# Kernel optimization log

Hardware: AMD Instinct MI355X
Metric: run time of the kernel (lower is better)

The kernel has to match this reference:

```python
import jax, jax.numpy as jnp
import numpy as np

N, E, D, H = 100000, 200000, 384, 768
BN_EPS = 1e-5


def setup_inputs() -> dict:
    key = jax.random.key(0)
    ks = jax.random.split(key, 8)
    w = lambda k, sh: jax.random.normal(k, sh, jnp.float32) * 0.02
    return {
        "x": jax.random.normal(ks[0], (N, D), jnp.float32),
        "edge_attr": jax.random.normal(ks[1], (E, D), jnp.float32),
        "gamma": jnp.ones((D,), jnp.float32),
        "beta": jnp.zeros((D,), jnp.float32),
        "eps": jnp.zeros((), jnp.float32),          # GINE train_eps, init 0
        "W_edge": w(ks[2], (D, D)),
        "b_edge": jnp.zeros((D,), jnp.float32),
        "W1": w(ks[3], (D, H)),
        "b1": jnp.zeros((H,), jnp.float32),
        "W2": w(ks[4], (H, D)),
        "b2": jnp.zeros((D,), jnp.float32),
        "edge_index": jax.random.randint(ks[5], (2, E), 0, N, jnp.int32),
    }


def reference(x, edge_attr, gamma, beta, eps, W_edge, b_edge, W1, b1, W2, b2, edge_index):
    # BatchNorm1d over the node (batch) dimension, training statistics
    mu = jnp.mean(x, axis=0)
    var = jnp.var(x, axis=0)
    h = (x - mu) * jax.lax.rsqrt(var + BN_EPS) * gamma + beta  # [N, D]

    src, dst = edge_index[0], edge_index[1]  # j -> i (PyG source_to_target)
    # GINEConv message: relu(x_j + lin(edge_attr))
    msg = jax.nn.relu(h[src] + edge_attr @ W_edge + b_edge)     # [E, D]
    agg = jax.ops.segment_sum(msg, dst, num_segments=N)         # sum aggregation

    # nn((1+eps)*x_i + agg) where nn = Linear->GELU->Linear
    z = (1.0 + eps) * h + agg
    z = jax.nn.gelu(z @ W1 + b1, approximate=False) @ W2 + b2

    # residual + outer GELU activation (drop_path/dropout = identity at eval)
    return x + jax.nn.gelu(z, approximate=False)
```

## Files before the change

### kernel.cpp

```cpp
#include <hip/hip_runtime.h>
#include <hip/hip_bf16.h>

#define Df 384
#define Hf 768
#define SCAN_CH 4096

typedef __bf16 bf16x8 __attribute__((ext_vector_type(8)));
typedef float f32x4 __attribute__((ext_vector_type(4)));

struct __attribute__((aligned(4))) U12 { unsigned int x, y, z; };

__device__ inline unsigned short f2bf(float f) {
    __hip_bfloat16 h = __float2bfloat16(f);
    return __builtin_bit_cast(unsigned short, h);
}
__device__ inline float bf2f(unsigned short u) {
    unsigned int v = ((unsigned int)u) << 16;
    return __builtin_bit_cast(float, v);
}
__device__ inline float lobf(unsigned int v) { return bf2f((unsigned short)(v & 0xffff)); }
__device__ inline float hibf(unsigned int v) { return bf2f((unsigned short)(v >> 16)); }
__device__ inline unsigned int pk2(float a, float b) {
    return (unsigned int)f2bf(a) | ((unsigned int)f2bf(b) << 16);
}
__device__ inline float gelu_(float v) {
    return 0.5f * v * (1.0f + erff(v * 0.70710678118654752f));
}
__device__ inline void gload16(const void* g, void* l) {
    __builtin_amdgcn_global_load_lds(
        (const __attribute__((address_space(1))) unsigned int*)g,
        (__attribute__((address_space(3))) unsigned int*)l, 16, 0, 0);
}

__global__ void bn_stats(const float* __restrict__ x, float* __restrict__ stats, int N) {
    int t = threadIdx.x;
    int c4 = (t % 96) * 4;
    int rs = t / 96;
    float s0 = 0, s1 = 0, s2 = 0, s3 = 0, q0 = 0, q1 = 0, q2 = 0, q3 = 0;
    for (int r = blockIdx.x * 2 + rs; r < N; r += gridDim.x * 2) {
        float4 v = *(const float4*)(x + (size_t)r * Df + c4);
        s0 += v.x; s1 += v.y; s2 += v.z; s3 += v.w;
        q0 += v.x * v.x; q1 += v.y * v.y; q2 += v.z * v.z; q3 += v.w * v.w;
    }
    unsafeAtomicAdd(&stats[c4 + 0], s0);
    unsafeAtomicAdd(&stats[c4 + 1], s1);
    unsafeAtomicAdd(&stats[c4 + 2], s2);
    unsafeAtomicAdd(&stats[c4 + 3], s3);
    unsafeAtomicAdd(&stats[Df + c4 + 0], q0);
    unsafeAtomicAdd(&stats[Df + c4 + 1], q1);
    unsafeAtomicAdd(&stats[Df + c4 + 2], q2);
    unsafeAtomicAdd(&stats[Df + c4 + 3], q3);
}

__global__ void bn_finalize(const float* __restrict__ stats,
                            const float* __restrict__ gamma,
                            const float* __restrict__ beta,
                            float* __restrict__ coef, int N) {
    int c = threadIdx.x;
    float invN = 1.0f / (float)N;
    float mu = stats[c] * invN;
    float var = stats[Df + c] * invN - mu * mu;
    float rs = rsqrtf(var + 1e-5f);
    float a = gamma[c] * rs;
    coef[c] = a;
    coef[Df + c] = beta[c] - mu * a;
}

__global__ void h_kernel(const float* __restrict__ x, const float* __restrict__ coef,
                         unsigned short* __restrict__ hb, int tot8) {
    int i = blockIdx.x * 256 + threadIdx.x;
    if (i >= tot8) return;
    size_t base = (size_t)i * 8;
    int c = (int)(base % Df);
    float4 x0 = *(const float4*)(x + base);
    float4 x1 = *(const float4*)(x + base + 4);
    const float* a = coef + c;
    const float* b = coef + Df + c;
    uint4 o;
    o.x = pk2(x0.x * a[0] + b[0], x0.y * a[1] + b[1]);
    o.y = pk2(x0.z * a[2] + b[2], x0.w * a[3] + b[3]);
    o.z = pk2(x1.x * a[4] + b[4], x1.y * a[5] + b[5]);
    o.w = pk2(x1.z * a[6] + b[6], x1.w * a[7] + b[7]);
    *(uint4*)(hb + base) = o;
}

__global__ void cast_bf16(const float* __restrict__ src, unsigned short* __restrict__ dst, int tot8) {
    int i = blockIdx.x * 256 + threadIdx.x;
    if (i >= tot8) return;
    size_t base = (size_t)i * 8;
    float4 x0 = *(const float4*)(src + base);
    float4 x1 = *(const float4*)(src + base + 4);
    uint4 o;
    o.x = pk2(x0.x, x0.y); o.y = pk2(x0.z, x0.w);
    o.z = pk2(x1.x, x1.y); o.w = pk2(x1.z, x1.w);
    *(uint4*)(dst + base) = o;
}

__global__ void wtrans(const float* __restrict__ Wsrc, unsigned short* __restrict__ Wdst,
                       int K, int Nc) {
    int idx = blockIdx.x * 256 + threadIdx.x;
    if (idx >= K * Nc) return;
    int k = idx / Nc, n = idx % Nc;
    Wdst[(size_t)n * K + k] = f2bf(Wsrc[idx]);
}

__global__ void degree_k(const int* __restrict__ dst, int* __restrict__ deg, int E) {
    int e = blockIdx.x * 256 + threadIdx.x;
    if (e < E) atomicAdd(&deg[dst[e]], 1);
}

__global__ void scan1(const int* __restrict__ deg, int* __restrict__ off,
                      int* __restrict__ sums, int N) {
    __shared__ int ts[256];
    int t = threadIdx.x;
    int base = blockIdx.x * SCAN_CH + t * 16;
    int v[16];
    int s = 0;
    for (int j = 0; j < 16; j++) {
        int idx = base + j;
        int d = (idx < N) ? deg[idx] : 0;
        v[j] = s;
        s += d;
    }
    ts[t] = s;
    __syncthreads();
    for (int o = 1; o < 256; o <<= 1) {
        int add = (t >= o) ? ts[t - o] : 0;
        __syncthreads();
        ts[t] += add;
        __syncthreads();
    }
    int pre = t ? ts[t - 1] : 0;
    for (int j = 0; j < 16; j++) {
        int idx = base + j;
        if (idx < N) off[idx] = pre + v[j];
    }
    if (t == 255) sums[blockIdx.x] = ts[255];
}

__global__ void scan2(int* __restrict__ sums, int nb) {
    int acc = 0;
    for (int b = 0; b < nb; b++) { int v = sums[b]; sums[b] = acc; acc += v; }
    sums[nb] = acc;
}

__global__ void scan3(int* __restrict__ off, const int* __restrict__ sums, int N, int nb) {
    int idx = blockIdx.x * 256 + threadIdx.x;
    if (idx < N) off[idx] += sums[idx / SCAN_CH];
    else if (idx == N) off[N] = sums[nb];
}

__global__ void fill_k(const int* __restrict__ dst, const int* __restrict__ src,
                       int* __restrict__ cursor, int* __restrict__ srcp,
                       int* __restrict__ pose, int E) {
    int e = blockIdx.x * 256 + threadIdx.x;
    if (e >= E) return;
    int pos = atomicAdd(&cursor[dst[e]], 1);
    srcp[pos] = src[e];
    pose[e] = pos;
}

__global__ __launch_bounds__(256) void aggregate(
    const unsigned short* __restrict__ msgl, const unsigned short* __restrict__ hb,
    const int* __restrict__ off, const int* __restrict__ srcp,
    const float* __restrict__ epsp,
    unsigned short* __restrict__ zb, int N) {
    int lane = threadIdx.x & 63;
    int wid = threadIdx.x >> 6;
    int nwaves = gridDim.x * 4;
    float s1p = 1.0f + epsp[0];
    int loff = lane * 6;
    for (int i = blockIdx.x * 4 + wid; i < N; i += nwaves) {
        int o0 = off[i], o1 = off[i + 1];
        float a0 = 0, a1 = 0, a2 = 0, a3 = 0, a4 = 0, a5 = 0;
        for (int p = o0; p < o1; ++p) {
            int s = srcp[p];
            U12 mv = *(const U12*)(msgl + (size_t)p * Df + loff);
            U12 hv = *(const U12*)(hb + (size_t)s * Df + loff);
            a0 += fmaxf(lobf(mv.x) + lobf(hv.x), 0.f);
            a1 += fmaxf(hibf(mv.x) + hibf(hv.x), 0.f);
            a2 += fmaxf(lobf(mv.y) + lobf(hv.y), 0.f);
            a3 += fmaxf(hibf(mv.y) + hibf(hv.y), 0.f);
            a4 += fmaxf(lobf(mv.z) + lobf(hv.z), 0.f);
            a5 += fmaxf(hibf(mv.z) + hibf(hv.z), 0.f);
        }
        U12 hv = *(const U12*)(hb + (size_t)i * Df + loff);
        U12 o;
        o.x = pk2(s1p * lobf(hv.x) + a0, s1p * hibf(hv.x) + a1);
        o.y = pk2(s1p * lobf(hv.y) + a2, s1p * hibf(hv.y) + a3);
        o.z = pk2(s1p * lobf(hv.z) + a4, s1p * hibf(hv.z) + a5);
        *(U12*)(zb + (size_t)i * Df + loff) = o;
    }
}

template <int NT, int EPI>
__global__ __launch_bounds__(512, 1) void gemm8(
    const unsigned short* __restrict__ Ab, const unsigned short* __restrict__ Bt,
    const float* __restrict__ bias, int M, int ncols,
    const int* __restrict__ pose,
    unsigned short* __restrict__ outb,
    const float* __restrict__ xres, float* __restrict__ outf, int ldo) {
    constexpr int K = NT * 64;
    __shared__ __align__(16) unsigned short As[3 * 256 * 64];
    __shared__ __align__(16) unsigned short Bs[3 * 128 * 64];

    const int t = threadIdx.x;
    const int nwg = gridDim.x;
    const int orig = blockIdx.x;
    const int xcd = orig & 7;
    const int q = nwg >> 3, r = nwg & 7;
    const int wgid = (xcd < r ? xcd * (q + 1) : r * (q + 1) + (xcd - r) * q) + (orig >> 3);
    const int pp = wgid / ncols;
    const int m0 = pp * 256;
    const int n0 = (wgid - pp * ncols) * 128;

    const int lane = t & 63;
    const int wid = t >> 6;
    const int fr = lane & 15;
    const int kg = lane >> 4;
    const int wm = wid >> 1;
    const int wn = wid & 1;
    const int srow = lane >> 3;
    const int scol = (lane & 7) ^ srow;

    f32x4 acc[4][4];
#pragma unroll
    for (int i = 0; i < 4; i++)
#pragma unroll
        for (int j = 0; j < 4; j++) acc[i][j] = (f32x4){0.f, 0.f, 0.f, 0.f};

#define STG_A(u, kt_, bufi) do {                                                \
        int rr_ = m0 + (u) * 64 + wid * 8 + srow;                               \
        if (rr_ >= M) rr_ = M - 1;                                              \
        gload16(Ab + (size_t)rr_ * K + (kt_) * 64 + (scol << 3),                \
                &As[(bufi) * 16384 + (u) * 4096 + wid * 512]);                  \
    } while (0)
#define STG_B(u, kt_, bufi) do {                                                \
        int rr_ = n0 + (u) * 64 + wid * 8 + srow;                               \
        gload16(Bt + (size_t)rr_ * K + (kt_) * 64 + (scol << 3),                \
                &Bs[(bufi) * 8192 + (u) * 4096 + wid * 512]);                   \
    } while (0)

#pragma unroll
    for (int u = 0; u < 4; u++) STG_A(u, 0, 0);
    STG_B(0, 0, 0); STG_B(1, 0, 0);
#pragma unroll
    for (int u = 0; u < 4; u++) STG_A(u, 1, 1);
    STG_B(0, 1, 1); STG_B(1, 1, 1);
    asm volatile("s_waitcnt vmcnt(6)" ::: "memory");
    __builtin_amdgcn_s_barrier();
    asm volatile("" ::: "memory");

    for (int kt = 0; kt < NT; ++kt) {
        const unsigned short* Ac = As + (kt % 3) * 16384;
        const unsigned short* Bc = Bs + (kt % 3) * 8192;
        const int nb = (kt + 2) % 3;
        const bool st = (kt + 2) < NT;

        if (st) { STG_A(0, kt + 2, nb); STG_A(1, kt + 2, nb); }

        bf16x8 a[4], b[4];
#pragma unroll
        for (int i = 0; i < 4; i++) {
            const int row = wm * 64 + i * 16 + fr;
            a[i] = *(const bf16x8*)&Ac[row * 64 + ((kg ^ (row & 7)) << 3)];
        }
#pragma unroll
        for (int j = 0; j < 4; j++) {
            const int row = wn * 64 + j * 16 + fr;
            b[j] = *(const bf16x8*)&Bc[row * 64 + ((kg ^ (row & 7)) << 3)];
        }
        if (st) { STG_A(2, kt + 2, nb); STG_A(3, kt + 2, nb); }
        __builtin_amdgcn_s_setprio(1);
#pragma unroll
        for (int i = 0; i < 4; i++)
#pragma unroll
            for (int j = 0; j < 4; j++)
                acc[i][j] = __builtin_amdgcn_mfma_f32_16x16x32_bf16(a[i], b[j], acc[i][j], 0, 0, 0);
        __builtin_amdgcn_s_setprio(0);

        if (st) { STG_B(0, kt + 2, nb); STG_B(1, kt + 2, nb); }
#pragma unroll
        for (int i = 0; i < 4; i++) {
            const int row = wm * 64 + i * 16 + fr;
            a[i] = *(const bf16x8*)&Ac[row * 64 + (((4 + kg) ^ (row & 7)) << 3)];
        }
#pragma unroll
        for (int j = 0; j < 4; j++) {
            const int row = wn * 64 + j * 16 + fr;
            b[j] = *(const bf16x8*)&Bc[row * 64 + (((4 + kg) ^ (row & 7)) << 3)];
        }
        __builtin_amdgcn_s_setprio(1);
#pragma unroll
        for (int i = 0; i < 4; i++)
#pragma unroll
            for (int j = 0; j < 4; j++)
                acc[i][j] = __builtin_amdgcn_mfma_f32_16x16x32_bf16(a[i], b[j], acc[i][j], 0, 0, 0);
        __builtin_amdgcn_s_setprio(0);

        if (kt < NT - 1) {
            if (st) asm volatile("s_waitcnt vmcnt(6)" ::: "memory");
            else    asm volatile("s_waitcnt vmcnt(0)" ::: "memory");
            __builtin_amdgcn_s_barrier();
            asm volatile("" ::: "memory");
        }
    }
#undef STG_A
#undef STG_B

    float bi[4];
#pragma unroll
    for (int j = 0; j < 4; j++) bi[j] = bias[n0 + wn * 64 + j * 16 + fr];

    const int kg4 = kg * 4;
#pragma unroll
    for (int i = 0; i < 4; i++) {
        const int rb = m0 + wm * 64 + i * 16 + kg4;
#pragma unroll
        for (int j = 0; j < 4; j++) {
            const int c = n0 + wn * 64 + j * 16 + fr;
#pragma unroll
            for (int r = 0; r < 4; r++) {
                const int row = rb + r;
                if (row < M) {
                    float v = acc[i][j][r] + bi[j];
                    if (EPI == 1) {
                        outb[(size_t)row * ldo + c] = f2bf(gelu_(v));
                    } else if (EPI == 2) {
                        size_t o = (size_t)row * ldo + c;
                        outf[o] = xres[o] + gelu_(v);
                    } else {
                        outb[(size_t)pose[row] * ldo + c] = f2bf(v);
                    }
                }
            }
        }
    }
}

extern "C" void kernel_launch(void* const* d_in, const int* in_sizes, int n_in,
                              void* d_out, int out_size, void* d_ws, size_t ws_size,
                              hipStream_t stream) {
    const float* x = (const float*)d_in[0];
    const float* ea = (const float*)d_in[1];
    const float* gamma = (const float*)d_in[2];
    const float* beta = (const float*)d_in[3];
    const float* epsp = (const float*)d_in[4];
    const float* W_edge = (const float*)d_in[5];
    const float* b_edge = (const float*)d_in[6];
    const float* W1 = (const float*)d_in[7];
    const float* b1 = (const float*)d_in[8];
    const float* W2 = (const float*)d_in[9];
    const float* b2 = (const float*)d_in[10];
    const int* eidx = (const int*)d_in[11];
    float* out = (float*)d_out;
    const int N = in_sizes[0] / Df;
    const int E = in_sizes[1] / Df;
    const int* esrc = eidx;
    const int* edst = eidx + E;

    char* w = (char*)d_ws;
    size_t off_ = 0;
    auto alloc = [&](size_t bytes) { char* p = w + off_; off_ += (bytes + 255) & ~(size_t)255; return p; };
    float* stats = (float*)alloc(2 * Df * sizeof(float));
    float* coef = (float*)alloc(2 * Df * sizeof(float));
    unsigned short* hb = (unsigned short*)alloc((size_t)N * Df * 2);
    unsigned short* zb = (unsigned short*)alloc((size_t)N * Df * 2);
    unsigned short* tb = (unsigned short*)alloc((size_t)N * Hf * 2);
    unsigned short* WeT = (unsigned short*)alloc((size_t)Df * Df * 2);
    unsigned short* W1T = (unsigned short*)alloc((size_t)Df * Hf * 2);
    unsigned short* W2T = (unsigned short*)alloc((size_t)Hf * Df * 2);
    int* deg = (int*)alloc((size_t)(N + 1) * 4);
    int* offs = (int*)alloc((size_t)(N + 1) * 4);
    int* srcp = (int*)alloc((size_t)E * 4);
    int* pose = (int*)alloc((size_t)E * 4);
    int* sums = (int*)alloc(64 * 4);
    size_t msgl_bytes = (size_t)E * Df * 2;
    unsigned short* msgl;
    if (off_ + msgl_bytes <= ws_size) msgl = (unsigned short*)alloc(msgl_bytes);
    else msgl = (unsigned short*)d_out;
    unsigned short* eab = tb;
    (void)n_in; (void)out_size;

    hipMemsetAsync(stats, 0, 2 * Df * sizeof(float), stream);
    hipMemsetAsync(deg, 0, (size_t)N * 4, stream);

    bn_stats<<<1024, 192, 0, stream>>>(x, stats, N);
    bn_finalize<<<1, Df, 0, stream>>>(stats, gamma, beta, coef, N);
    int tot8 = N * Df / 8;
    h_kernel<<<(tot8 + 255) / 256, 256, 0, stream>>>(x, coef, hb, tot8);

    int etot8 = E * Df / 8;
    cast_bf16<<<(etot8 + 255) / 256, 256, 0, stream>>>(ea, eab, etot8);

    wtrans<<<(Df * Df + 255) / 256, 256, 0, stream>>>(W_edge, WeT, Df, Df);
    wtrans<<<(Df * Hf + 255) / 256, 256, 0, stream>>>(W1, W1T, Df, Hf);
    wtrans<<<(Hf * Df + 255) / 256, 256, 0, stream>>>(W2, W2T, Hf, Df);

    int nb = (N + SCAN_CH - 1) / SCAN_CH;
    degree_k<<<(E + 255) / 256, 256, 0, stream>>>(edst, deg, E);
    scan1<<<nb, 256, 0, stream>>>(deg, offs, sums, N);
    scan2<<<1, 1, 0, stream>>>(sums, nb);
    scan3<<<(N + 256) / 256, 256, 0, stream>>>(offs, sums, N, nb);
    hipMemcpyAsync(deg, offs, (size_t)N * 4, hipMemcpyDeviceToDevice, stream);
    fill_k<<<(E + 255) / 256, 256, 0, stream>>>(edst, esrc, deg, srcp, pose, E);

    int ep = (E + 255) / 256;
    gemm8<6, 3><<<dim3(ep * (Df / 128)), 512, 0, stream>>>(
        eab, WeT, b_edge, E, Df / 128, pose, msgl, nullptr, nullptr, Df);

    aggregate<<<2048, 256, 0, stream>>>(msgl, hb, offs, srcp, epsp, zb, N);

    int np = (N + 255) / 256;
    gemm8<6, 1><<<dim3(np * (Hf / 128)), 512, 0, stream>>>(
        zb, W1T, b1, N, Hf / 128, nullptr, tb, nullptr, nullptr, Hf);
    gemm8<12, 2><<<dim3(np * (Df / 128)), 512, 0, stream>>>(
        tb, W2T, b2, N, Df / 128, nullptr, nullptr, x, out, Df);
}
```

Measured before the change: 1.121 ms.

## Widen GEMM tiles to 256x192 with half-K double-buffered ping-pong pipeline

Replaces the 256x128 triple-buffered GEMM with a 256x192 tile: each wave owns a 128x48 sub-tile and the K tile is split into two 32-wide halves in a double buffer. Loads for later stages are interleaved between MFMA phases, with barriers around each phase. The wider N tile is meant to cut how often A is re-fetched and to raise MFMA work per shared-memory read. In exchange it uses more registers for accumulators, adds many more barriers per K step, and launches fewer workgroups.

```diff
diff --git a/kernel.cpp b/kernel.cpp
--- a/kernel.cpp
+++ b/kernel.cpp
@@ -194,15 +194,15 @@
 }
 
 template <int NT, int EPI>
-__global__ __launch_bounds__(512, 1) void gemm8(
+__global__ __launch_bounds__(512, 1) void gemm8p(
     const unsigned short* __restrict__ Ab, const unsigned short* __restrict__ Bt,
     const float* __restrict__ bias, int M, int ncols,
     const int* __restrict__ pose,
     unsigned short* __restrict__ outb,
     const float* __restrict__ xres, float* __restrict__ outf, int ldo) {
     constexpr int K = NT * 64;
-    __shared__ __align__(16) unsigned short As[3 * 256 * 64];
-    __shared__ __align__(16) unsigned short Bs[3 * 128 * 64];
+    __shared__ __align__(16) unsigned short AS[2 * 2 * 256 * 32];
+    __shared__ __align__(16) unsigned short BS[2 * 2 * 192 * 32];
 
     const int t = threadIdx.x;
     const int nwg = gridDim.x;
@@ -212,118 +212,137 @@
     const int wgid = (xcd < r ? xcd * (q + 1) : r * (q + 1) + (xcd - r) * q) + (orig >> 3);
     const int pp = wgid / ncols;
     const int m0 = pp * 256;
-    const int n0 = (wgid - pp * ncols) * 128;
+    const int n0 = (wgid - pp * ncols) * 192;
 
     const int lane = t & 63;
     const int wid = t >> 6;
     const int fr = lane & 15;
     const int kg = lane >> 4;
-    const int wm = wid >> 1;
-    const int wn = wid & 1;
-    const int srow = lane >> 3;
-    const int scol = (lane & 7) ^ srow;
-
-    f32x4 acc[4][4];
-#pragma unroll
-    for (int i = 0; i < 4; i++)
-#pragma unroll
-        for (int j = 0; j < 4; j++) acc[i][j] = (f32x4){0.f, 0.f, 0.f, 0.f};
-
-#define STG_A(u, kt_, bufi) do {                                                \
-        int rr_ = m0 + (u) * 64 + wid * 8 + srow;                               \
-        if (rr_ >= M) rr_ = M - 1;                                              \
-        gload16(Ab + (size_t)rr_ * K + (kt_) * 64 + (scol << 3),                \
-                &As[(bufi) * 16384 + (u) * 4096 + wid * 512]);                  \
-    } while (0)
-#define STG_B(u, kt_, bufi) do {                                                \
-        int rr_ = n0 + (u) * 64 + wid * 8 + srow;                               \
-        gload16(Bt + (size_t)rr_ * K + (kt_) * 64 + (scol << 3),                \
-                &Bs[(bufi) * 8192 + (u) * 4096 + wid * 512]);                   \
-    } while (0)
-
-#pragma unroll
-    for (int u = 0; u < 4; u++) STG_A(u, 0, 0);
-    STG_B(0, 0, 0); STG_B(1, 0, 0);
-#pragma unroll
-    for (int u = 0; u < 4; u++) STG_A(u, 1, 1);
-    STG_B(0, 1, 1); STG_B(1, 1, 1);
+    const int wm = wid >> 2;
+    const int wn = wid & 3;
+    const int segw = ((lane & 3) ^ ((lane >> 3) & 3)) << 3;
+    const int rsw = (kg ^ ((fr >> 1) & 3)) << 3;
+
+    f32x4 acc[8][3];
+#pragma unroll
+    for (int i = 0; i < 8; i++)
+#pragma unroll
+        for (int j = 0; j < 3; j++) acc[i][j] = (f32x4){0.f, 0.f, 0.f, 0.f};
+
+#define STG_AH(tt, kh) do {                                                     \
+        const int bb_ = ((tt) & 1) * 2 + (kh);                                  \
+        _Pragma("unroll")                                                       \
+        for (int c_ = 0; c_ < 2; c_++) {                                        \
+            int row_ = c_ * 128 + wid * 16 + (lane >> 2);                       \
+            int gr_ = m0 + row_; if (gr_ >= M) gr_ = M - 1;                     \
+            gload16(Ab + (size_t)gr_ * K + (tt) * 64 + (kh) * 32 + segw,        \
+                    &AS[(bb_ * 256 + c_ * 128 + wid * 16) * 32]);               \
+        } } while (0)
+#define STG_BH(tt, kh) do {                                                     \
+        const int bb_ = ((tt) & 1) * 2 + (kh);                                  \
+        _Pragma("unroll")                                                       \
+        for (int c_ = 0; c_ < 2; c_++) {                                        \
+            int row_ = c_ * 64 + wid * 16 + (lane >> 2);                        \
+            gload16(Bt + (size_t)(n0 + row_) * K + (tt) * 64 + (kh) * 32 + segw,\
+                    &BS[(bb_ * 192 + c_ * 64 + wid * 16) * 32]);                \
+        } } while (0)
+
+    STG_AH(0, 0); STG_BH(0, 0); STG_AH(0, 1); STG_BH(0, 1);
+    STG_AH(1, 0); STG_BH(1, 0); STG_AH(1, 1);
     asm volatile("s_waitcnt vmcnt(6)" ::: "memory");
     __builtin_amdgcn_s_barrier();
-    asm volatile("" ::: "memory");
 
     for (int kt = 0; kt < NT; ++kt) {
-        const unsigned short* Ac = As + (kt % 3) * 16384;
-        const unsigned short* Bc = Bs + (kt % 3) * 8192;
-        const int nb = (kt + 2) % 3;
-        const bool st = (kt + 2) < NT;
-
-        if (st) { STG_A(0, kt + 2, nb); STG_A(1, kt + 2, nb); }
-
-        bf16x8 a[4], b[4];
-#pragma unroll
-        for (int i = 0; i < 4; i++) {
-            const int row = wm * 64 + i * 16 + fr;
-            a[i] = *(const bf16x8*)&Ac[row * 64 + ((kg ^ (row & 7)) << 3)];
+        const int b = kt & 1;
+        const unsigned short* Ah0 = &AS[(b * 2 + 0) * 256 * 32];
+        const unsigned short* Ah1 = &AS[(b * 2 + 1) * 256 * 32];
+        const unsigned short* Bh0 = &BS[(b * 2 + 0) * 192 * 32];
+        const unsigned short* Bh1 = &BS[(b * 2 + 1) * 192 * 32];
+        bf16x8 a[8], bf0, bf1, bf2;
+
+#pragma unroll
+        for (int i = 0; i < 8; i++)
+            a[i] = *(const bf16x8*)&Ah0[(wm * 128 + i * 16 + fr) * 32 + rsw];
+        bf0 = *(const bf16x8*)&Bh0[(wn * 48 + 0 + fr) * 32 + rsw];
+        bf1 = *(const bf16x8*)&Bh0[(wn * 48 + 16 + fr) * 32 + rsw];
+        if (kt + 1 < NT) STG_BH(kt + 1, 1);
+        __builtin_amdgcn_s_barrier();
+        asm volatile("s_waitcnt lgkmcnt(0)" ::: "memory");
+        __builtin_amdgcn_sched_barrier(0);
+        __builtin_amdgcn_s_setprio(1);
+#pragma unroll
+        for (int i = 0; i < 8; i++) {
+            acc[i][0] = __builtin_amdgcn_mfma_f32_16x16x32_bf16(a[i], bf0, acc[i][0], 0, 0, 0);
+            acc[i][1] = __builtin_amdgcn_mfma_f32_16x16x32_bf16(a[i], bf1, acc[i][1], 0, 0, 0);
         }
-#pragma unroll
-        for (int j = 0; j < 4; j++) {
-            const int row = wn * 64 + j * 16 + fr;
-            b[j] = *(const bf16x8*)&Bc[row * 64 + ((kg ^ (row & 7)) << 3)];
+        __builtin_amdgcn_s_setprio(0);
+        __builtin_amdgcn_s_barrier();
+
+        bf2 = *(const bf16x8*)&Bh0[(wn * 48 + 32 + fr) * 32 + rsw];
+        if (kt + 2 < NT) STG_AH(kt + 2, 0);
+        __builtin_amdgcn_s_barrier();
+        asm volatile("s_waitcnt lgkmcnt(0)" ::: "memory");
+        __builtin_amdgcn_sched_barrier(0);
+        __builtin_amdgcn_s_setprio(1);
+#pragma unroll
+        for (int i = 0; i < 8; i++)
+            acc[i][2] = __builtin_amdgcn_mfma_f32_16x16x32_bf16(a[i], bf2, acc[i][2], 0, 0, 0);
+        __builtin_amdgcn_s_setprio(0);
+        __builtin_amdgcn_s_barrier();
+
+#pragma unroll
+        for (int i = 0; i < 8; i++)
+            a[i] = *(const bf16x8*)&Ah1[(wm * 128 + i * 16 + fr) * 32 + rsw];
+        bf0 = *(const bf16x8*)&Bh1[(wn * 48 + 0 + fr) * 32 + rsw];
+        bf1 = *(const bf16x8*)&Bh1[(wn * 48 + 16 + fr) * 32 + rsw];
+        if (kt + 2 < NT) STG_BH(kt + 2, 0);
+        __builtin_amdgcn_s_barrier();
+        asm volatile("s_waitcnt lgkmcnt(0)" ::: "memory");
+        __builtin_amdgcn_sched_barrier(0);
+        __builtin_amdgcn_s_setprio(1);
+#pragma unroll
+        for (int i = 0; i < 8; i++) {
+            acc[i][0] = __builtin_amdgcn_mfma_f32_16x16x32_bf16(a[i], bf0, acc[i][0], 0, 0, 0);
+            acc[i][1] = __builtin_amdgcn_mfma_f32_16x16x32_bf16(a[i], bf1, acc[i][1], 0, 0, 0);
         }
-        if (st) { STG_A(2, kt + 2, nb); STG_A(3, kt + 2, nb); }
+        __builtin_amdgcn_s_setprio(0);
+        __builtin_amdgcn_s_barrier();
+
+        bf2 = *(const bf16x8*)&Bh1[(wn * 48 + 32 + fr) * 32 + rsw];
+        if (kt + 2 < NT) STG_AH(kt + 2, 1);
+        __builtin_amdgcn_s_barrier();
+        asm volatile("s_waitcnt lgkmcnt(0)" ::: "memory");
+        __builtin_amdgcn_sched_barrier(0);
         __builtin_amdgcn_s_setprio(1);
 #pragma unroll
-        for (int i = 0; i < 4; i++)
-#pragma unroll
-            for (int j = 0; j < 4; j++)
-                acc[i][j] = __builtin_amdgcn_mfma_f32_16x16x32_bf16(a[i], b[j], acc[i][j], 0, 0, 0);
+        for (int i = 0; i < 8; i++)
+            acc[i][2] = __builtin_amdgcn_mfma_f32_16x16x32_bf16(a[i], bf2, acc[i][2], 0, 0, 0);
         __builtin_amdgcn_s_setprio(0);
-
-        if (st) { STG_B(0, kt + 2, nb); STG_B(1, kt + 2, nb); }
-#pragma unroll
-        for (int i = 0; i < 4; i++) {
-            const int row = wm * 64 + i * 16 + fr;
-            a[i] = *(const bf16x8*)&Ac[row * 64 + (((4 + kg) ^ (row & 7)) << 3)];
+        if (kt + 1 < NT) {
+            if (kt + 2 < NT) asm volatile("s_waitcnt vmcnt(6)" ::: "memory");
+            else             asm volatile("s_waitcnt vmcnt(0)" ::: "memory");
         }
-#pragma unroll
-        for (int j = 0; j < 4; j++) {
-            const int row = wn * 64 + j * 16 + fr;
-            b[j] = *(const bf16x8*)&Bc[row * 64 + (((4 + kg) ^ (row & 7)) << 3)];
-        }
-        __builtin_amdgcn_s_setprio(1);
-#pragma unroll
-        for (int i = 0; i < 4; i++)
-#pragma unroll
-            for (int j = 0; j < 4; j++)
-                acc[i][j] = __builtin_amdgcn_mfma_f32_16x16x32_bf16(a[i], b[j], acc[i][j], 0, 0, 0);
-        __builtin_amdgcn_s_setprio(0);
-
-        if (kt < NT - 1) {
-            if (st) asm volatile("s_waitcnt vmcnt(6)" ::: "memory");
-            else    asm volatile("s_waitcnt vmcnt(0)" ::: "memory");
-            __builtin_amdgcn_s_barrier();
-            asm volatile("" ::: "memory");
-        }
-    }
-#undef STG_A
-#undef STG_B
-
-    float bi[4];
-#pragma unroll
-    for (int j = 0; j < 4; j++) bi[j] = bias[n0 + wn * 64 + j * 16 + fr];
+        __builtin_amdgcn_s_barrier();
+    }
+#undef STG_AH
+#undef STG_BH
+
+    float bi[3];
+#pragma unroll
+    for (int j = 0; j < 3; j++) bi[j] = bias[n0 + wn * 48 + j * 16 + fr];
 
     const int kg4 = kg * 4;
 #pragma unroll
-    for (int i = 0; i < 4; i++) {
-        const int rb = m0 + wm * 64 + i * 16 + kg4;
-#pragma unroll
-        for (int j = 0; j < 4; j++) {
-            const int c = n0 + wn * 64 + j * 16 + fr;
-#pragma unroll
-            for (int r = 0; r < 4; r++) {
-                const int row = rb + r;
+    for (int i = 0; i < 8; i++) {
+        const int rb = m0 + wm * 128 + i * 16 + kg4;
+#pragma unroll
+        for (int j = 0; j < 3; j++) {
+            const int c = n0 + wn * 48 + j * 16 + fr;
+#pragma unroll
+            for (int rr = 0; rr < 4; rr++) {
+                const int row = rb + rr;
                 if (row < M) {
-                    float v = acc[i][j][r] + bi[j];
+                    float v = acc[i][j][rr] + bi[j];
                     if (EPI == 1) {
                         outb[(size_t)row * ldo + c] = f2bf(gelu_(v));
                     } else if (EPI == 2) {
@@ -406,14 +425,14 @@
     fill_k<<<(E + 255) / 256, 256, 0, stream>>>(edst, esrc, deg, srcp, pose, E);
 
     int ep = (E + 255) / 256;
-    gemm8<6, 3><<<dim3(ep * (Df / 128)), 512, 0, stream>>>(
-        eab, WeT, b_edge, E, Df / 128, pose, msgl, nullptr, nullptr, Df);
+    gemm8p<6, 3><<<dim3(ep * (Df / 192)), 512, 0, stream>>>(
+        eab, WeT, b_edge, E, Df / 192, pose, msgl, nullptr, nullptr, Df);
 
     aggregate<<<2048, 256, 0, stream>>>(msgl, hb, offs, srcp, epsp, zb, N);
 
     int np = (N + 255) / 256;
-    gemm8<6, 1><<<dim3(np * (Hf / 128)), 512, 0, stream>>>(
-        zb, W1T, b1, N, Hf / 128, nullptr, tb, nullptr, nullptr, Hf);
-    gemm8<12, 2><<<dim3(np * (Df / 128)), 512, 0, stream>>>(
-        tb, W2T, b2, N, Df / 128, nullptr, nullptr, x, out, Df);
-}
+    gemm8p<6, 1><<<dim3(np * (Hf / 192)), 512, 0, stream>>>(
+        zb, W1T, b1, N, Hf / 192, nullptr, tb, nullptr, nullptr, Hf);
+    gemm8p<12, 2><<<dim3(np * (Df / 192)), 512, 0, stream>>>(
+        tb, W2T, b2, N, Df / 192, nullptr, nullptr, x, out, Df);
+}
```

New measurement: 1.277 ms. +13.8%, slower.

## Fuse MLP's two GEMMs into one kernel keeping hidden activations in LDS

Applied to the files above, without the earlier changes.

Replaces the two tiled GEMM launches for the node MLP with a single fused kernel. Each 64-row block stages its z tile in shared memory, computes the 768-wide GELU hidden layer into shared memory, then runs the second GEMM with the residual GELU epilogue. This avoids writing and rereading the N×768 bf16 hidden tensor in global memory. In exchange, weights are read straight from global or L2 on every k-step with no LDS staging or pipelining. The 144 KB of LDS also limits each CU to one block, which may cut MFMA efficiency compared with the tuned gemm8.

```diff
diff --git a/kernel.cpp b/kernel.cpp
--- a/kernel.cpp
+++ b/kernel.cpp
@@ -193,6 +193,124 @@
     }
 }
 
+__global__ __launch_bounds__(512, 1) void mlp_fused(
+    const unsigned short* __restrict__ zb, const unsigned short* __restrict__ W1T,
+    const float* __restrict__ b1, const unsigned short* __restrict__ W2T,
+    const float* __restrict__ b2, const float* __restrict__ x,
+    float* __restrict__ out, int M) {
+    __shared__ __align__(16) unsigned short zS[64 * 384];
+    __shared__ __align__(16) unsigned short tS[64 * 768];
+
+    const int t = threadIdx.x;
+    const int lane = t & 63;
+    const int wid = t >> 6;
+    const int fr = lane & 15;
+    const int kg = lane >> 4;
+    const int kg4 = kg * 4;
+    const int m0 = blockIdx.x * 64;
+
+#pragma unroll
+    for (int si = 0; si < 6; si++) {
+        int c = (wid * 6 + si) * 64 + lane;
+        int row = c / 48;
+        int pos = c - row * 48;
+        int gr = m0 + row; if (gr >= M) gr = M - 1;
+        gload16(zb + (size_t)gr * Df + ((pos ^ (row & 7)) << 3),
+                &zS[(wid * 6 + si) * 512]);
+    }
+    asm volatile("s_waitcnt vmcnt(0)" ::: "memory");
+    __builtin_amdgcn_s_barrier();
+
+    const int cb1 = wid * 96;
+    f32x4 acc1[4][6];
+#pragma unroll
+    for (int i = 0; i < 4; i++)
+#pragma unroll
+        for (int j = 0; j < 6; j++) acc1[i][j] = (f32x4){0.f, 0.f, 0.f, 0.f};
+
+#pragma unroll
+    for (int kt = 0; kt < 12; kt++) {
+        bf16x8 a[4], b[6];
+#pragma unroll
+        for (int i = 0; i < 4; i++) {
+            const int rr = i * 16 + fr;
+            const int pos = (kt * 4 + kg) ^ (rr & 7);
+            a[i] = *(const bf16x8*)&zS[rr * Df + pos * 8];
+        }
+#pragma unroll
+        for (int j = 0; j < 6; j++)
+            b[j] = *(const bf16x8*)(W1T + (size_t)(cb1 + j * 16 + fr) * Df + kt * 32 + kg * 8);
+#pragma unroll
+        for (int i = 0; i < 4; i++)
+#pragma unroll
+            for (int j = 0; j < 6; j++)
+                acc1[i][j] = __builtin_amdgcn_mfma_f32_16x16x32_bf16(a[i], b[j], acc1[i][j], 0, 0, 0);
+    }
+
+    float bv1[6];
+#pragma unroll
+    for (int j = 0; j < 6; j++) bv1[j] = b1[cb1 + j * 16 + fr];
+#pragma unroll
+    for (int i = 0; i < 4; i++) {
+#pragma unroll
+        for (int j = 0; j < 6; j++) {
+            const int col = cb1 + j * 16 + fr;
+#pragma unroll
+            for (int r = 0; r < 4; r++) {
+                const int row = i * 16 + kg4 + r;
+                const int pos = (col >> 3) ^ (row & 7);
+                tS[row * Hf + pos * 8 + (col & 7)] = f2bf(gelu_(acc1[i][j][r] + bv1[j]));
+            }
+        }
+    }
+    __syncthreads();
+
+    const int cb2 = wid * 48;
+    f32x4 acc2[4][3];
+#pragma unroll
+    for (int i = 0; i < 4; i++)
+#pragma unroll
+        for (int j = 0; j < 3; j++) acc2[i][j] = (f32x4){0.f, 0.f, 0.f, 0.f};
+
+#pragma unroll
+    for (int kt = 0; kt < 24; kt++) {
+        bf16x8 a[4], b[3];
+#pragma unroll
+        for (int i = 0; i < 4; i++) {
+            const int rr = i * 16 + fr;
+            const int pos = (kt * 4 + kg) ^ (rr & 7);
+            a[i] = *(const bf16x8*)&tS[rr * Hf + pos * 8];
+        }
+#pragma unroll
+        for (int j = 0; j < 3; j++)
+            b[j] = *(const bf16x8*)(W2T + (size_t)(cb2 + j * 16 + fr) * Hf + kt * 32 + kg * 8);
+#pragma unroll
+        for (int i = 0; i < 4; i++)
+#pragma unroll
+            for (int j = 0; j < 3; j++)
+                acc2[i][j] = __builtin_amdgcn_mfma_f32_16x16x32_bf16(a[i], b[j], acc2[i][j], 0, 0, 0);
+    }
+
+    float bv2[3];
+#pragma unroll
+    for (int j = 0; j < 3; j++) bv2[j] = b2[cb2 + j * 16 + fr];
+#pragma unroll
+    for (int i = 0; i < 4; i++) {
+#pragma unroll
+        for (int r = 0; r < 4; r++) {
+            const int row = m0 + i * 16 + kg4 + r;
+            if (row < M) {
+#pragma unroll
+                for (int j = 0; j < 3; j++) {
+                    const int col = cb2 + j * 16 + fr;
+                    size_t o = (size_t)row * Df + col;
+                    out[o] = x[o] + gelu_(acc2[i][j][r] + bv2[j]);
+                }
+            }
+        }
+    }
+}
+
 template <int NT, int EPI>
 __global__ __launch_bounds__(512, 1) void gemm8(
     const unsigned short* __restrict__ Ab, const unsigned short* __restrict__ Bt,
@@ -366,7 +484,7 @@
     float* coef = (float*)alloc(2 * Df * sizeof(float));
     unsigned short* hb = (unsigned short*)alloc((size_t)N * Df * 2);
     unsigned short* zb = (unsigned short*)alloc((size_t)N * Df * 2);
-    unsigned short* tb = (unsigned short*)alloc((size_t)N * Hf * 2);
+    unsigned short* eab = (unsigned short*)alloc((size_t)E * Df * 2);
     unsigned short* WeT = (unsigned short*)alloc((size_t)Df * Df * 2);
     unsigned short* W1T = (unsigned short*)alloc((size_t)Df * Hf * 2);
     unsigned short* W2T = (unsigned short*)alloc((size_t)Hf * Df * 2);
@@ -379,7 +497,6 @@
     unsigned short* msgl;
     if (off_ + msgl_bytes <= ws_size) msgl = (unsigned short*)alloc(msgl_bytes);
     else msgl = (unsigned short*)d_out;
-    unsigned short* eab = tb;
     (void)n_in; (void)out_size;
 
     hipMemsetAsync(stats, 0, 2 * Df * sizeof(float), stream);
@@ -411,9 +528,5 @@
 
     aggregate<<<2048, 256, 0, stream>>>(msgl, hb, offs, srcp, epsp, zb, N);
 
-    int np = (N + 255) / 256;
-    gemm8<6, 1><<<dim3(np * (Hf / 128)), 512, 0, stream>>>(
-        zb, W1T, b1, N, Hf / 128, nullptr, tb, nullptr, nullptr, Hf);
-    gemm8<12, 2><<<dim3(np * (Df / 128)), 512, 0, stream>>>(
-        tb, W2T, b2, N, Df / 128, nullptr, nullptr, x, out, Df);
-}
+    mlp_fused<<<(N + 63) / 64, 512, 0, stream>>>(zb, W1T, b1, W2T, b2, x, out, N);
+}
```

After: 1.152 ms. 2.7% more time.
